# Kernel tuning notes

Measured on AMD Instinct MI355X. Metric: run time of the kernel, lower is better.

## Reference

```python
import jax, jax.numpy as jnp
import numpy as np

# RoIAlign config (matches init_kwargs)
OUT_H, OUT_W = 7, 7
SPATIAL_SCALE = 0.25
SAMPLE_NUM = 2  # sampling points per bin side (static)


def setup_inputs() -> dict:
    key = jax.random.key(0)
    k0, k1, k2, k3 = jax.random.split(key, 4)
    B, C, H, W = 2, 256, 200, 336
    N = 1024
    img_h, img_w = H / SPATIAL_SCALE, W / SPATIAL_SCALE
    features = jax.random.normal(k0, (B, C, H, W), dtype=jnp.float32)
    # build valid rois: [batch_idx, x1, y1, x2, y2] in image coordinates
    bidx = jax.random.randint(k1, (N,), 0, B).astype(jnp.float32)
    ctr = jax.random.uniform(k2, (N, 2)) * jnp.array([img_w, img_h], jnp.float32)
    wh = (0.05 + 0.35 * jax.random.uniform(k3, (N, 2))) * jnp.array([img_w, img_h], jnp.float32)
    x1y1 = jnp.clip(ctr - wh / 2, 0.0)
    x2y2 = jnp.minimum(ctr + wh / 2, jnp.array([img_w, img_h], jnp.float32))
    rois = jnp.concatenate([bidx[:, None], x1y1[:, 0:1], x1y1[:, 1:2], x2y2[:, 0:1], x2y2[:, 1:2]], axis=1)
    return {"features": features, "rois": rois}


def _roi_align(features, rois):
    B, C, H, W = features.shape
    N = rois.shape[0]
    ns = SAMPLE_NUM
    P, Q = OUT_H * ns, OUT_W * ns  # full sampling grid per roi

    bidx = rois[:, 0].astype(jnp.int32)
    x1 = rois[:, 1] * SPATIAL_SCALE
    y1 = rois[:, 2] * SPATIAL_SCALE
    x2 = rois[:, 3] * SPATIAL_SCALE
    y2 = rois[:, 4] * SPATIAL_SCALE
    roi_w = jnp.maximum(x2 - x1, 1.0)  # aligned=False legacy semantics
    roi_h = jnp.maximum(y2 - y1, 1.0)
    bin_w = roi_w / OUT_W
    bin_h = roi_h / OUT_H

    # sample coords: y = y1 + (p + 0.5) * bin_h / ns, p in [0, P)
    ys = y1[:, None] + (jnp.arange(P, dtype=jnp.float32) + 0.5) * (bin_h[:, None] / ns)  # (N,P)
    xs = x1[:, None] + (jnp.arange(Q, dtype=jnp.float32) + 0.5) * (bin_w[:, None] / ns)  # (N,Q)

    # out-of-bound samples contribute zero (kernel skips y<-1 or y>H)
    ymask = (ys >= -1.0) & (ys <= H)
    xmask = (xs >= -1.0) & (xs <= W)
    y = jnp.clip(ys, 0.0, H - 1)
    x = jnp.clip(xs, 0.0, W - 1)
    y0 = jnp.floor(y).astype(jnp.int32)
    x0 = jnp.floor(x).astype(jnp.int32)
    y1i = jnp.minimum(y0 + 1, H - 1)
    x1i = jnp.minimum(x0 + 1, W - 1)
    ly = y - y0.astype(jnp.float32)
    lx = x - x0.astype(jnp.float32)
    hy, hx = 1.0 - ly, 1.0 - lx

    b = bidx[:, None, None]            # (N,1,1)
    def gather(yi, xi):                # -> (N,P,Q,C)
        return features[b, :, yi[:, :, None], xi[:, None, :]]
    f00 = gather(y0, x0)
    f01 = gather(y0, x1i)
    f10 = gather(y1i, x0)
    f11 = gather(y1i, x1i)

    wy0, wy1 = hy[:, :, None, None], ly[:, :, None, None]  # (N,P,1,1)
    wx0, wx1 = hx[:, None, :, None], lx[:, None, :, None]  # (N,1,Q,1)
    val = wy0 * (wx0 * f00 + wx1 * f01) + wy1 * (wx0 * f10 + wx1 * f11)
    val = val * (ymask[:, :, None, None] & xmask[:, None, :, None])

    # average the ns x ns samples per output bin
    val = val.reshape(N, OUT_H, ns, OUT_W, ns, C).mean(axis=(2, 4))  # (N,OUT_H,OUT_W,C)
    return jnp.transpose(val, (0, 3, 1, 2))  # (N,C,OUT_H,OUT_W)


def reference(features, rois):
    return _roi_align(features, rois)
```

## Files before the change

kernel.cpp:

```cpp
#include <hip/hip_runtime.h>
#include <hip/hip_fp16.h>

#define BB   2
#define CCH  256
#define HH   200
#define WW   336
#define HWN  (HH * WW)
#define OH   7
#define OW   7
#define SCALEF 0.25f
#define NBIN (OH * OW)
#define PER_ROI (CCH * NBIN)

typedef float  nfloat4 __attribute__((ext_vector_type(4)));

__device__ __forceinline__ __half2 u32_as_h2(unsigned int u) {
    union { unsigned int u; __half2 h; } c;
    c.u = u;
    return c.h;
}

__global__ __launch_bounds__(256) void transpose_f16_k(const float* __restrict__ src,
                                                       unsigned short* __restrict__ dst) {
    __shared__ float tile[64][65];
    const int b   = blockIdx.z;
    const int hw0 = blockIdx.x * 64;
    const int c0  = blockIdx.y * 64;
    const int tx  = threadIdx.x;
    const int ty  = threadIdx.y;

#pragma unroll
    for (int r = 0; r < 4; ++r) {
        const int cl = ty + r * 16;
        const nfloat4 v = __builtin_nontemporal_load(
            (const nfloat4*)(src + (size_t)(b * CCH + c0 + cl) * HWN + hw0 + tx * 4));
        tile[cl][tx * 4 + 0] = v.x;
        tile[cl][tx * 4 + 1] = v.y;
        tile[cl][tx * 4 + 2] = v.z;
        tile[cl][tx * 4 + 3] = v.w;
    }
    __syncthreads();
#pragma unroll
    for (int r = 0; r < 4; ++r) {
        const int hwl = ty + r * 16;
        ushort4 o;
        o.x = __half_as_ushort(__float2half(tile[tx * 4 + 0][hwl]));
        o.y = __half_as_ushort(__float2half(tile[tx * 4 + 1][hwl]));
        o.z = __half_as_ushort(__float2half(tile[tx * 4 + 2][hwl]));
        o.w = __half_as_ushort(__float2half(tile[tx * 4 + 3][hwl]));
        *(ushort4*)(dst + (size_t)(b * HWN + hw0 + hwl) * CCH + c0 + tx * 4) = o;
    }
}

__global__ __launch_bounds__(512) void roi_align_f16_k(const unsigned short* __restrict__ f,
                                                       const float* __restrict__ rois,
                                                       float* __restrict__ out) {
    const int n    = blockIdx.x;
    const int tid  = threadIdx.x;
    const int lane = tid & 63;
    const int g    = tid >> 6;
    const int c4   = lane * 4;

    __shared__ __align__(16) float buf[PER_ROI];
    __shared__ int   s_yb0[14], s_yb1[14];
    __shared__ int   s_xb0[14], s_xb1[14];
    __shared__ float s_ly[14],  s_lx[14];
    __shared__ float s_vy[14],  s_vx[14];

    const float* r = rois + n * 5;
    const int   b   = (int)r[0];
    const float rx1 = r[1] * SCALEF, ry1 = r[2] * SCALEF;
    const float rx2 = r[3] * SCALEF, ry2 = r[4] * SCALEF;
    const float bw = fmaxf(rx2 - rx1, 1.0f) * (1.0f / OW);
    const float bh = fmaxf(ry2 - ry1, 1.0f) * (1.0f / OH);

    if (tid < 14) {
        const float ys = ry1 + ((float)tid + 0.5f) * (bh * 0.5f);
        s_vy[tid] = (ys >= -1.0f && ys <= (float)HH) ? 1.0f : 0.0f;
        const float y = fminf(fmaxf(ys, 0.0f), (float)(HH - 1));
        const int y0  = (int)floorf(y);
        const int y1  = min(y0 + 1, HH - 1);
        s_yb0[tid] = (b * HH + y0) * (WW * CCH);
        s_yb1[tid] = (b * HH + y1) * (WW * CCH);
        s_ly[tid]  = y - (float)y0;
    } else if (tid >= 64 && tid < 78) {
        const int j = tid - 64;
        const float xs = rx1 + ((float)j + 0.5f) * (bw * 0.5f);
        s_vx[j] = (xs >= -1.0f && xs <= (float)WW) ? 1.0f : 0.0f;
        const float x = fminf(fmaxf(xs, 0.0f), (float)(WW - 1));
        const int x0  = (int)floorf(x);
        const int x1  = min(x0 + 1, WW - 1);
        s_xb0[j] = x0 * CCH;
        s_xb1[j] = x1 * CCH;
        s_lx[j]  = x - (float)x0;
    }
    __syncthreads();

    const unsigned short* fb = f + c4;

    for (int bin = g; bin < NBIN; bin += 8) {
        const int ph = bin / OW;
        const int pw = bin - ph * OW;
        float accx = 0.0f, accy = 0.0f, accz = 0.0f, accw = 0.0f;
#pragma unroll
        for (int ix = 0; ix < 2; ++ix) {
            const int px  = pw * 2 + ix;
            const int xb0 = s_xb0[px], xb1 = s_xb1[px];
            const float lx = s_lx[px];
            const float mv = s_vx[px] * 0.25f;
            const __half2 HX = __float2half2_rn(1.0f - lx);
            const __half2 LX = __float2half2_rn(lx);
#pragma unroll
            for (int iy = 0; iy < 2; ++iy) {
                const int py  = ph * 2 + iy;
                const int yb0 = s_yb0[py], yb1 = s_yb1[py];
                const float ly = s_ly[py];
                const float m  = mv * s_vy[py];
                const uint2 q00 = *(const uint2*)(fb + yb0 + xb0);
                const uint2 q01 = *(const uint2*)(fb + yb0 + xb1);
                const uint2 q10 = *(const uint2*)(fb + yb1 + xb0);
                const uint2 q11 = *(const uint2*)(fb + yb1 + xb1);
                const __half2 r0a = __hfma2(LX, u32_as_h2(q01.x), __hmul2(HX, u32_as_h2(q00.x)));
                const __half2 r0b = __hfma2(LX, u32_as_h2(q01.y), __hmul2(HX, u32_as_h2(q00.y)));
                const __half2 r1a = __hfma2(LX, u32_as_h2(q11.x), __hmul2(HX, u32_as_h2(q10.x)));
                const __half2 r1b = __hfma2(LX, u32_as_h2(q11.y), __hmul2(HX, u32_as_h2(q10.y)));
                const __half2 MH0 = __float2half2_rn(m * (1.0f - ly));
                const __half2 MH1 = __float2half2_rn(m * ly);
                const __half2 vA = __hfma2(MH1, r1a, __hmul2(MH0, r0a));
                const __half2 vB = __hfma2(MH1, r1b, __hmul2(MH0, r0b));
                accx += __low2float(vA);
                accy += __high2float(vA);
                accz += __low2float(vB);
                accw += __high2float(vB);
            }
        }
        buf[(c4 + 0) * NBIN + bin] = accx;
        buf[(c4 + 1) * NBIN + bin] = accy;
        buf[(c4 + 2) * NBIN + bin] = accz;
        buf[(c4 + 3) * NBIN + bin] = accw;
    }
    __syncthreads();

    nfloat4* ob = (nfloat4*)(out + (size_t)n * PER_ROI);
    const nfloat4* bb4 = (const nfloat4*)buf;
    for (int i = tid; i < PER_ROI / 4; i += 512) {
        __builtin_nontemporal_store(bb4[i], ob + i);
    }
}

__global__ __launch_bounds__(256) void roi_align_direct_k(const float* __restrict__ f,
                                                          const float* __restrict__ rois,
                                                          float* __restrict__ out) {
    const int n   = blockIdx.x;
    const int c   = threadIdx.x;

    __shared__ int   s_y0[14], s_y1[14], s_x0[14], s_x1[14];
    __shared__ float s_ly[14], s_lx[14], s_vy[14], s_vx[14];

    const float* r = rois + n * 5;
    const int   b   = (int)r[0];
    const float rx1 = r[1] * SCALEF, ry1 = r[2] * SCALEF;
    const float rx2 = r[3] * SCALEF, ry2 = r[4] * SCALEF;
    const float bw = fmaxf(rx2 - rx1, 1.0f) * (1.0f / OW);
    const float bh = fmaxf(ry2 - ry1, 1.0f) * (1.0f / OH);

    if (c < 14) {
        const float ys = ry1 + ((float)c + 0.5f) * (bh * 0.5f);
        s_vy[c] = (ys >= -1.0f && ys <= (float)HH) ? 1.0f : 0.0f;
        const float y = fminf(fmaxf(ys, 0.0f), (float)(HH - 1));
        const int y0  = (int)floorf(y);
        s_y0[c] = y0 * WW;
        s_y1[c] = min(y0 + 1, HH - 1) * WW;
        s_ly[c] = y - (float)y0;
    } else if (c >= 64 && c < 78) {
        const int j = c - 64;
        const float xs = rx1 + ((float)j + 0.5f) * (bw * 0.5f);
        s_vx[j] = (xs >= -1.0f && xs <= (float)WW) ? 1.0f : 0.0f;
        const float x = fminf(fmaxf(xs, 0.0f), (float)(WW - 1));
        const int x0  = (int)floorf(x);
        s_x0[j] = x0;
        s_x1[j] = min(x0 + 1, WW - 1);
        s_lx[j] = x - (float)x0;
    }
    __syncthreads();

    const float* fb = f + (size_t)(b * CCH + c) * HWN;
    for (int bin = 0; bin < NBIN; ++bin) {
        const int ph = bin / OW, pw = bin - ph * OW;
        float acc = 0.0f;
        for (int iy = 0; iy < 2; ++iy) {
            const int py = ph * 2 + iy;
            const float ly = s_ly[py], hy = 1.0f - ly;
            for (int ix = 0; ix < 2; ++ix) {
                const int px = pw * 2 + ix;
                const float lx = s_lx[px], hx = 1.0f - lx;
                const float m = s_vy[py] * s_vx[px] * 0.25f;
                acc += m * (hy * (hx * fb[s_y0[py] + s_x0[px]] + lx * fb[s_y0[py] + s_x1[px]]) +
                            ly * (hx * fb[s_y1[py] + s_x0[px]] + lx * fb[s_y1[py] + s_x1[px]]));
            }
        }
        out[(size_t)n * PER_ROI + c * NBIN + bin] = acc;
    }
}

extern "C" void kernel_launch(void* const* d_in, const int* in_sizes, int n_in,
                              void* d_out, int out_size, void* d_ws, size_t ws_size,
                              hipStream_t stream) {
    const float* feat = (const float*)d_in[0];
    const float* rois = (const float*)d_in[1];
    float* out = (float*)d_out;
    const int N = in_sizes[1] / 5;

    const size_t need = (size_t)BB * CCH * HWN * sizeof(unsigned short);
    if (ws_size >= need) {
        unsigned short* fcl = (unsigned short*)d_ws;
        transpose_f16_k<<<dim3(HWN / 64, CCH / 64, BB), dim3(16, 16), 0, stream>>>(feat, fcl);
        roi_align_f16_k<<<N, 512, 0, stream>>>(fcl, rois, out);
    } else {
        roi_align_direct_k<<<N, 256, 0, stream>>>(feat, rois, out);
    }
}
```

Baseline: 258.5 us.

## Sort RoIs by batch and vertical band, remap blocks across XCDs, shrink LDS buffer

Adds a single-block counting-sort kernel that buckets RoIs by batch index and vertical band of the feature map, producing a permutation. The align kernel remaps block IDs so each group of blocks (assumed to land on one XCD via round-robin dispatch) handles spatially nearby RoIs, aiming to improve L2 reuse of the transposed feature map. The staging buffer in LDS is changed from fp32 to fp16, halving shared memory so more blocks fit per CU (launch bounds now request 8 waves-per-EU occupancy). The cost is an extra serial launch and an extra fp16 rounding of outputs before they are written as fp32.

```diff
diff --git a/kernel.cpp b/kernel.cpp
--- a/kernel.cpp
+++ b/kernel.cpp
@@ -11,6 +11,8 @@
 #define SCALEF 0.25f
 #define NBIN (OH * OW)
 #define PER_ROI (CCH * NBIN)
+#define NBANDS 8
+#define NBUCK (BB * NBANDS)
 
 typedef float  nfloat4 __attribute__((ext_vector_type(4)));
 
@@ -18,6 +20,39 @@
     union { unsigned int u; __half2 h; } c;
     c.u = u;
     return c.h;
+}
+
+__global__ __launch_bounds__(1024) void roi_sort_k(const float* __restrict__ rois,
+                                                   int N, int* __restrict__ perm) {
+    const int tid = threadIdx.x;
+    if (N > 1024 || N < 8) {
+        for (int i = tid; i < N; i += blockDim.x) perm[i] = i;
+        return;
+    }
+    __shared__ int cnt[NBUCK], off[NBUCK];
+    __shared__ unsigned char keys[1024];
+    if (tid < NBUCK) cnt[tid] = 0;
+    __syncthreads();
+    for (int i = tid; i < N; i += blockDim.x) {
+        const float* r = rois + i * 5;
+        const int b = (int)r[0];
+        const float yc = (r[2] + r[4]) * 0.5f * SCALEF;
+        int band = (int)(yc * ((float)NBANDS / (float)HH));
+        band = min(max(band, 0), NBANDS - 1);
+        const int k = b * NBANDS + band;
+        keys[i] = (unsigned char)k;
+        atomicAdd(&cnt[k], 1);
+    }
+    __syncthreads();
+    if (tid == 0) {
+        int s = 0;
+        for (int k = 0; k < NBUCK; ++k) { off[k] = s; s += cnt[k]; }
+    }
+    __syncthreads();
+    for (int i = tid; i < N; i += blockDim.x) {
+        const int pos = atomicAdd(&off[keys[i]], 1);
+        perm[pos] = i;
+    }
 }
 
 __global__ __launch_bounds__(256) void transpose_f16_k(const float* __restrict__ src,
@@ -52,16 +87,24 @@
     }
 }
 
-__global__ __launch_bounds__(512) void roi_align_f16_k(const unsigned short* __restrict__ f,
-                                                       const float* __restrict__ rois,
-                                                       float* __restrict__ out) {
-    const int n    = blockIdx.x;
+__global__ __launch_bounds__(512, 8) void roi_align_f16_k(const unsigned short* __restrict__ f,
+                                                          const float* __restrict__ rois,
+                                                          const int* __restrict__ perm,
+                                                          float* __restrict__ out) {
+    const int nblk = gridDim.x;
+    int p;
+    if ((nblk & 7) == 0) {
+        p = (blockIdx.x & 7) * (nblk >> 3) + (blockIdx.x >> 3);
+    } else {
+        p = blockIdx.x;
+    }
+    const int n    = perm[p];
     const int tid  = threadIdx.x;
     const int lane = tid & 63;
     const int g    = tid >> 6;
     const int c4   = lane * 4;
 
-    __shared__ __align__(16) float buf[PER_ROI];
+    __shared__ __align__(16) unsigned short buf_h[PER_ROI];
     __shared__ int   s_yb0[14], s_yb1[14];
     __shared__ int   s_xb0[14], s_xb1[14];
     __shared__ float s_ly[14],  s_lx[14];
@@ -134,17 +177,22 @@
                 accw += __high2float(vB);
             }
         }
-        buf[(c4 + 0) * NBIN + bin] = accx;
-        buf[(c4 + 1) * NBIN + bin] = accy;
-        buf[(c4 + 2) * NBIN + bin] = accz;
-        buf[(c4 + 3) * NBIN + bin] = accw;
+        buf_h[(c4 + 0) * NBIN + bin] = __half_as_ushort(__float2half(accx));
+        buf_h[(c4 + 1) * NBIN + bin] = __half_as_ushort(__float2half(accy));
+        buf_h[(c4 + 2) * NBIN + bin] = __half_as_ushort(__float2half(accz));
+        buf_h[(c4 + 3) * NBIN + bin] = __half_as_ushort(__float2half(accw));
     }
     __syncthreads();
 
     nfloat4* ob = (nfloat4*)(out + (size_t)n * PER_ROI);
-    const nfloat4* bb4 = (const nfloat4*)buf;
+    const uint2* bb = (const uint2*)buf_h;
     for (int i = tid; i < PER_ROI / 4; i += 512) {
-        __builtin_nontemporal_store(bb4[i], ob + i);
+        const uint2 q = bb[i];
+        const __half2 a = u32_as_h2(q.x), c = u32_as_h2(q.y);
+        nfloat4 v;
+        v.x = __low2float(a);  v.y = __high2float(a);
+        v.z = __low2float(c);  v.w = __high2float(c);
+        __builtin_nontemporal_store(v, ob + i);
     }
 }
 
@@ -211,11 +259,14 @@
     float* out = (float*)d_out;
     const int N = in_sizes[1] / 5;
 
-    const size_t need = (size_t)BB * CCH * HWN * sizeof(unsigned short);
+    const size_t tensor_bytes = (size_t)BB * CCH * HWN * sizeof(unsigned short);
+    const size_t need = tensor_bytes + (size_t)N * sizeof(int);
     if (ws_size >= need) {
         unsigned short* fcl = (unsigned short*)d_ws;
+        int* perm = (int*)((char*)d_ws + tensor_bytes);
+        roi_sort_k<<<1, 1024, 0, stream>>>(rois, N, perm);
         transpose_f16_k<<<dim3(HWN / 64, CCH / 64, BB), dim3(16, 16), 0, stream>>>(feat, fcl);
-        roi_align_f16_k<<<N, 512, 0, stream>>>(fcl, rois, out);
+        roi_align_f16_k<<<N, 512, 0, stream>>>(fcl, rois, perm, out);
     } else {
         roi_align_direct_k<<<N, 256, 0, stream>>>(feat, rois, out);
     }
```

Result: faster. 244.4 us (-5.4%).
